# Performance work log

Measured on AMD Instinct MI355X. Metric: run time of the kernel, lower is better.

Reference implementation:

```python
import jax, jax.numpy as jnp
import numpy as np

N, L, D = 4, 2048, 1024
H_DIM, OUT_DIM = 1024, 1024


def setup_inputs() -> dict:
    key = jax.random.key(0)
    ks = jax.random.split(key, 7)
    scale = 0.02
    return {
        "x": jax.random.normal(ks[0], (N, L, D), dtype=jnp.float32),
        "Wq": jax.random.normal(ks[1], (D, H_DIM), dtype=jnp.float32) * scale,
        "bq": jnp.zeros((H_DIM,), dtype=jnp.float32),
        "Wk": jax.random.normal(ks[2], (D, H_DIM), dtype=jnp.float32) * scale,
        "bk": jnp.zeros((H_DIM,), dtype=jnp.float32),
        "Wv": jax.random.normal(ks[3], (D, OUT_DIM), dtype=jnp.float32) * scale,
        "bv": jnp.zeros((OUT_DIM,), dtype=jnp.float32),
    }


def reference(x, Wq, bq, Wk, bk, Wv, bv):
    # q,k: [N,L,h_dim], v: [N,L,out_dim]
    q = jnp.einsum("nld,dh->nlh", x, Wq) + bq
    k = jnp.einsum("nld,dh->nlh", x, Wk) + bk
    v = jnp.einsum("nld,do->nlo", x, Wv) + bv
    # scores: [N,L,L]
    qk = jnp.einsum("nlh,nmh->nlm", q, k)
    # NOTE: original scales by sqrt(qk.shape[-1]) == sqrt(L) (seq len), not sqrt(h_dim)
    seq_len = qk.shape[-1]
    s = jax.nn.softmax(qk / jnp.sqrt(jnp.asarray(seq_len, dtype=qk.dtype)), axis=-1)
    return jnp.einsum("nlm,nmo->nlo", s, v)
```

## Files before the change

### kernel.cpp

```cpp
#include <hip/hip_runtime.h>
#include <hip/hip_bf16.h>


typedef __attribute__((ext_vector_type(8))) short bf16x8;
typedef __attribute__((ext_vector_type(4))) float f32x4;

#define AS_G(p) ((__attribute__((address_space(1))) void*)(p))
#define AS_L(p) ((__attribute__((address_space(3))) void*)(p))

__device__ __forceinline__ unsigned short f2bf(float f) {
  unsigned int u = __float_as_uint(f);
  unsigned int lsb = (u >> 16) & 1u;
  u += 0x7fffu + lsb;
  return (unsigned short)(u >> 16);
}

__device__ __forceinline__ float bf2f(unsigned short h) {
  return __uint_as_float(((unsigned int)h) << 16);
}


template <int EPI>
__global__ __launch_bounds__(256) void gemm64(
    const unsigned short* __restrict__ A, const unsigned short* __restrict__ B,
    float* __restrict__ C, long long sA, long long sB, long long sC,
    int K, int lda, int ldb, int ldc,
    unsigned short* __restrict__ qb, unsigned short* __restrict__ kb,
    unsigned short* __restrict__ vt,
    const float* __restrict__ bq, const float* __restrict__ bk_,
    const float* __restrict__ bv)
{
  __shared__ unsigned short lA[128 * 64];
  __shared__ unsigned short lB[128 * 64];

  const int t = threadIdx.x;
  const int rowBase = blockIdx.y * 128;
  const int colBase = blockIdx.x * 128;
  A += (long long)blockIdx.z * sA;
  B += (long long)blockIdx.z * sB;

  const int l = t & 63;
  const int w = t >> 6;
  const int wrow = (w >> 1) * 64;
  const int wcol = (w & 1) * 64;
  const int q = l >> 4;
  const int r16 = l & 15;

  f32x4 acc[4][4] = {};

  const int r0 = t >> 3;
  const int goff = (((t & 7) ^ (r0 & 7)) << 3);

  for (int kt = 0; kt < K; kt += 64) {
    __syncthreads();
#pragma unroll
    for (int u = 0; u < 4; u++) {
      const int row = r0 + 32 * u;
      __builtin_amdgcn_global_load_lds(AS_G(A + (size_t)(rowBase + row) * lda + kt + goff),
                                       AS_L(lA + (t + 256 * u) * 8), 16, 0, 0);
      __builtin_amdgcn_global_load_lds(AS_G(B + (size_t)(colBase + row) * ldb + kt + goff),
                                       AS_L(lB + (t + 256 * u) * 8), 16, 0, 0);
    }
    __syncthreads();

#pragma unroll
    for (int ks = 0; ks < 2; ks++) {
      bf16x8 af[4], bfr[4];
#pragma unroll
      for (int i = 0; i < 4; i++) {
        const int s = ((ks * 4 + q) ^ (r16 & 7));
        af[i] = *(const bf16x8*)(lA + (wrow + i * 16 + r16) * 64 + s * 8);
      }
#pragma unroll
      for (int j = 0; j < 4; j++) {
        const int s = ((ks * 4 + q) ^ (r16 & 7));
        bfr[j] = *(const bf16x8*)(lB + (wcol + j * 16 + r16) * 64 + s * 8);
      }
#pragma unroll
      for (int i = 0; i < 4; i++)
#pragma unroll
        for (int j = 0; j < 4; j++)
          acc[i][j] = __builtin_amdgcn_mfma_f32_16x16x32_bf16(af[i], bfr[j], acc[i][j], 0, 0, 0);
    }
  }

  if (EPI == 0) {
    C += (long long)blockIdx.z * sC;
#pragma unroll
    for (int i = 0; i < 4; i++) {
#pragma unroll
      for (int r = 0; r < 4; r++) {
        int row = rowBase + wrow + i * 16 + q * 4 + r;
#pragma unroll
        for (int j = 0; j < 4; j++) {
          int col = colBase + wcol + j * 16 + r16;
          C[(size_t)row * ldc + col] = acc[i][j][r];
        }
      }
    }
  } else {
    const int seg = colBase >> 10;
    if (seg < 2) {
      unsigned short* dst = seg ? kb : qb;
      const float* bias = seg ? bk_ : bq;
      const int cb = colBase & 1023;
#pragma unroll
      for (int i = 0; i < 4; i++) {
#pragma unroll
        for (int r = 0; r < 4; r++) {
          int row = rowBase + wrow + i * 16 + q * 4 + r;
#pragma unroll
          for (int j = 0; j < 4; j++) {
            int col = cb + wcol + j * 16 + r16;
            dst[(size_t)row * 1024 + col] = f2bf(acc[i][j][r] + bias[col]);
          }
        }
      }
    } else {
      const int ob = colBase - 2048;
#pragma unroll
      for (int i = 0; i < 4; i++) {
        int posBase = rowBase + wrow + i * 16 + q * 4;
        int b = posBase >> 11;
        int pos = posBase & 2047;
#pragma unroll
        for (int j = 0; j < 4; j++) {
          int o = ob + wcol + j * 16 + r16;
          float bias = bv[o];
          ushort4 pk;
          pk.x = f2bf(acc[i][j][0] + bias);
          pk.y = f2bf(acc[i][j][1] + bias);
          pk.z = f2bf(acc[i][j][2] + bias);
          pk.w = f2bf(acc[i][j][3] + bias);
          *(ushort4*)(vt + ((size_t)((b << 10) + o) * 2048 + pos)) = pk;
        }
      }
    }
  }
}


__global__ __launch_bounds__(256) void cast_f32_to_bf16(
    const float* __restrict__ in, unsigned short* __restrict__ out, int n4)
{
  int i = blockIdx.x * 256 + threadIdx.x;
  if (i >= n4) return;
  float4 v = ((const float4*)in)[i];
  ushort4 o;
  o.x = f2bf(v.x); o.y = f2bf(v.y); o.z = f2bf(v.z); o.w = f2bf(v.w);
  ((ushort4*)out)[i] = o;
}


__global__ __launch_bounds__(256) void wtrans(
    const float* __restrict__ Wq, const float* __restrict__ Wk,
    const float* __restrict__ Wv, unsigned short* __restrict__ WT)
{
  __shared__ float tile[32][33];
  const float* in = blockIdx.z == 0 ? Wq : (blockIdx.z == 1 ? Wk : Wv);
  unsigned short* out = WT + (size_t)blockIdx.z * 1024 * 1024;
  const int bc = blockIdx.x * 32;
  const int br = blockIdx.y * 32;
  const int tx = threadIdx.x;
  const int ty = threadIdx.y;
#pragma unroll
  for (int i = 0; i < 4; i++)
    tile[ty + i * 8][tx] = in[(size_t)(br + ty + i * 8) * 1024 + bc + tx];
  __syncthreads();
#pragma unroll
  for (int i = 0; i < 4; i++)
    out[(size_t)(bc + ty + i * 8) * 1024 + br + tx] = f2bf(tile[tx][ty + i * 8]);
}


__global__ __launch_bounds__(256) void softmax_rows(
    const float* __restrict__ S, unsigned short* __restrict__ P, float scale)
{
  const size_t row = blockIdx.x;
  const float* s = S + row * 2048;
  unsigned short* p = P + row * 2048;
  const int t = threadIdx.x;

  float v[8];
  float m = -1e30f;
#pragma unroll
  for (int i = 0; i < 8; i++) {
    v[i] = s[t + i * 256];
    m = fmaxf(m, v[i]);
  }
#pragma unroll
  for (int off = 32; off >= 1; off >>= 1) m = fmaxf(m, __shfl_xor(m, off));
  __shared__ float redm[4];
  if ((t & 63) == 0) redm[t >> 6] = m;
  __syncthreads();
  m = fmaxf(fmaxf(redm[0], redm[1]), fmaxf(redm[2], redm[3]));

  float e[8];
  float sum = 0.f;
#pragma unroll
  for (int i = 0; i < 8; i++) {
    e[i] = __expf((v[i] - m) * scale);
    sum += e[i];
  }
#pragma unroll
  for (int off = 32; off >= 1; off >>= 1) sum += __shfl_xor(sum, off);
  __shared__ float reds[4];
  if ((t & 63) == 0) reds[t >> 6] = sum;
  __syncthreads();
  sum = reds[0] + reds[1] + reds[2] + reds[3];
  float inv = 1.0f / sum;
#pragma unroll
  for (int i = 0; i < 8; i++) p[t + i * 256] = f2bf(e[i] * inv);
}


extern "C" void kernel_launch(void* const* d_in, const int* in_sizes, int n_in,
                              void* d_out, int out_size, void* d_ws, size_t ws_size,
                              hipStream_t stream) {
  (void)in_sizes; (void)n_in; (void)out_size;

  const float* x  = (const float*)d_in[0];
  const float* Wq = (const float*)d_in[1];
  const float* bq = (const float*)d_in[2];
  const float* Wk = (const float*)d_in[3];
  const float* bk = (const float*)d_in[4];
  const float* Wv = (const float*)d_in[5];
  const float* bv = (const float*)d_in[6];
  float* out = (float*)d_out;

  const int Nb = 4, L = 2048, D = 1024, H = 1024, O = 1024;
  const int M = Nb * L;
  const int NQKV = 3 * H;

  char* ws = (char*)d_ws;
  size_t off = 0;
  unsigned short* xb = (unsigned short*)(ws + off); off += (size_t)M * D * 2;
  unsigned short* qb = (unsigned short*)(ws + off); off += (size_t)M * H * 2;
  unsigned short* kb = (unsigned short*)(ws + off); off += (size_t)M * H * 2;
  unsigned short* vt = (unsigned short*)(ws + off); off += (size_t)M * O * 2;
  unsigned short* WT = (unsigned short*)(ws + off); off += (size_t)NQKV * D * 2;
  float* S = (float*)(ws + off); off += (size_t)Nb * L * L * 4;
  unsigned short* P = qb;
  if (ws_size < off) return;

  dim3 blk256(256);

  cast_f32_to_bf16<<<(M * D / 4 + 255) / 256, blk256, 0, stream>>>(x, xb, M * D / 4);

  wtrans<<<dim3(32, 32, 3), dim3(32, 8), 0, stream>>>(Wq, Wk, Wv, WT);

  gemm64<2><<<dim3(NQKV / 128, M / 128, 1), blk256, 0, stream>>>(
      xb, WT, nullptr, 0, 0, 0, D, D, D, 0, qb, kb, vt, bq, bk, bv);

  gemm64<0><<<dim3(L / 128, L / 128, Nb), blk256, 0, stream>>>(
      qb, kb, S, (long long)L * H, (long long)L * H, (long long)L * L,
      H, H, H, L, nullptr, nullptr, nullptr, nullptr, nullptr, nullptr);

  softmax_rows<<<Nb * L, blk256, 0, stream>>>(S, P, 0.022097086912079608f);

  gemm64<0><<<dim3(O / 128, L / 128, Nb), blk256, 0, stream>>>(
      P, vt, out, (long long)L * L, (long long)O * L, (long long)L * O,
      L, L, L, O, nullptr, nullptr, nullptr, nullptr, nullptr, nullptr);
}
```

Baseline: 276.5 us.

## Fuse softmax exp into QK GEMM epilogue and defer normalization to PV GEMM

The QK^T GEMM epilogue now computes exp(score*scale) directly, writes bf16 unnormalized probabilities, and accumulates per-row sums with atomics. The PV GEMM epilogue divides each output row by its sum. This removes the fp32 score matrix round trip and the separate softmax kernel. In exchange it drops the max-subtraction, so large scores could overflow exp, and it adds atomic contention on the row sums.

```diff
diff --git a/kernel.cpp b/kernel.cpp
--- a/kernel.cpp
+++ b/kernel.cpp
@@ -23,12 +23,13 @@
 template <int EPI>
 __global__ __launch_bounds__(256) void gemm64(
     const unsigned short* __restrict__ A, const unsigned short* __restrict__ B,
-    float* __restrict__ C, long long sA, long long sB, long long sC,
+    float* __restrict__ Cf, long long sA, long long sB, long long sC,
     int K, int lda, int ldb, int ldc,
-    unsigned short* __restrict__ qb, unsigned short* __restrict__ kb,
-    unsigned short* __restrict__ vt,
-    const float* __restrict__ bq, const float* __restrict__ bk_,
-    const float* __restrict__ bv)
+    unsigned short* __restrict__ u0, unsigned short* __restrict__ u1,
+    unsigned short* __restrict__ u2,
+    const float* __restrict__ f0, const float* __restrict__ f1,
+    const float* __restrict__ f2,
+    float* __restrict__ rsum, float scale)
 {
   __shared__ unsigned short lA[128 * 64];
   __shared__ unsigned short lB[128 * 64];
@@ -84,25 +85,32 @@
     }
   }
 
-  if (EPI == 0) {
-    C += (long long)blockIdx.z * sC;
+  if (EPI == 1) {
+    unsigned short* p16 = u0 + (long long)blockIdx.z * sC;
+    float* rs = rsum + (long long)blockIdx.z * 2048;
 #pragma unroll
     for (int i = 0; i < 4; i++) {
 #pragma unroll
       for (int r = 0; r < 4; r++) {
         int row = rowBase + wrow + i * 16 + q * 4 + r;
+        float rowpart = 0.f;
 #pragma unroll
         for (int j = 0; j < 4; j++) {
           int col = colBase + wcol + j * 16 + r16;
-          C[(size_t)row * ldc + col] = acc[i][j][r];
-        }
-      }
-    }
-  } else {
+          float e = __expf(acc[i][j][r] * scale);
+          p16[(size_t)row * ldc + col] = f2bf(e);
+          rowpart += e;
+        }
+#pragma unroll
+        for (int m = 1; m < 16; m <<= 1) rowpart += __shfl_xor(rowpart, m);
+        if (r16 == 0) atomicAdd(rs + row, rowpart);
+      }
+    }
+  } else if (EPI == 2) {
     const int seg = colBase >> 10;
     if (seg < 2) {
-      unsigned short* dst = seg ? kb : qb;
-      const float* bias = seg ? bk_ : bq;
+      unsigned short* dst = seg ? u1 : u0;
+      const float* bias = seg ? f1 : f0;
       const int cb = colBase & 1023;
 #pragma unroll
       for (int i = 0; i < 4; i++) {
@@ -126,13 +134,29 @@
 #pragma unroll
         for (int j = 0; j < 4; j++) {
           int o = ob + wcol + j * 16 + r16;
-          float bias = bv[o];
+          float bias = f2[o];
           ushort4 pk;
           pk.x = f2bf(acc[i][j][0] + bias);
           pk.y = f2bf(acc[i][j][1] + bias);
           pk.z = f2bf(acc[i][j][2] + bias);
           pk.w = f2bf(acc[i][j][3] + bias);
-          *(ushort4*)(vt + ((size_t)((b << 10) + o) * 2048 + pos)) = pk;
+          *(ushort4*)(u2 + ((size_t)((b << 10) + o) * 2048 + pos)) = pk;
+        }
+      }
+    }
+  } else {
+    float* C = Cf + (long long)blockIdx.z * sC;
+    const float* rs = rsum + (long long)blockIdx.z * 2048;
+#pragma unroll
+    for (int i = 0; i < 4; i++) {
+#pragma unroll
+      for (int r = 0; r < 4; r++) {
+        int row = rowBase + wrow + i * 16 + q * 4 + r;
+        float inv = 1.0f / rs[row];
+#pragma unroll
+        for (int j = 0; j < 4; j++) {
+          int col = colBase + wcol + j * 16 + r16;
+          C[(size_t)row * ldc + col] = acc[i][j][r] * inv;
         }
       }
     }
@@ -141,9 +165,11 @@
 
 
 __global__ __launch_bounds__(256) void cast_f32_to_bf16(
-    const float* __restrict__ in, unsigned short* __restrict__ out, int n4)
+    const float* __restrict__ in, unsigned short* __restrict__ out, int n4,
+    float* __restrict__ rzero, int nz4)
 {
   int i = blockIdx.x * 256 + threadIdx.x;
+  if (i < nz4) ((float4*)rzero)[i] = make_float4(0.f, 0.f, 0.f, 0.f);
   if (i >= n4) return;
   float4 v = ((const float4*)in)[i];
   ushort4 o;
@@ -173,47 +199,6 @@
 }
 
 
-__global__ __launch_bounds__(256) void softmax_rows(
-    const float* __restrict__ S, unsigned short* __restrict__ P, float scale)
-{
-  const size_t row = blockIdx.x;
-  const float* s = S + row * 2048;
-  unsigned short* p = P + row * 2048;
-  const int t = threadIdx.x;
-
-  float v[8];
-  float m = -1e30f;
-#pragma unroll
-  for (int i = 0; i < 8; i++) {
-    v[i] = s[t + i * 256];
-    m = fmaxf(m, v[i]);
-  }
-#pragma unroll
-  for (int off = 32; off >= 1; off >>= 1) m = fmaxf(m, __shfl_xor(m, off));
-  __shared__ float redm[4];
-  if ((t & 63) == 0) redm[t >> 6] = m;
-  __syncthreads();
-  m = fmaxf(fmaxf(redm[0], redm[1]), fmaxf(redm[2], redm[3]));
-
-  float e[8];
-  float sum = 0.f;
-#pragma unroll
-  for (int i = 0; i < 8; i++) {
-    e[i] = __expf((v[i] - m) * scale);
-    sum += e[i];
-  }
-#pragma unroll
-  for (int off = 32; off >= 1; off >>= 1) sum += __shfl_xor(sum, off);
-  __shared__ float reds[4];
-  if ((t & 63) == 0) reds[t >> 6] = sum;
-  __syncthreads();
-  sum = reds[0] + reds[1] + reds[2] + reds[3];
-  float inv = 1.0f / sum;
-#pragma unroll
-  for (int i = 0; i < 8; i++) p[t + i * 256] = f2bf(e[i] * inv);
-}
-
-
 extern "C" void kernel_launch(void* const* d_in, const int* in_sizes, int n_in,
                               void* d_out, int out_size, void* d_ws, size_t ws_size,
                               hipStream_t stream) {
@@ -239,26 +224,30 @@
   unsigned short* kb = (unsigned short*)(ws + off); off += (size_t)M * H * 2;
   unsigned short* vt = (unsigned short*)(ws + off); off += (size_t)M * O * 2;
   unsigned short* WT = (unsigned short*)(ws + off); off += (size_t)NQKV * D * 2;
-  float* S = (float*)(ws + off); off += (size_t)Nb * L * L * 4;
-  unsigned short* P = qb;
+  unsigned short* P  = (unsigned short*)(ws + off); off += (size_t)Nb * L * L * 2;
+  float* rsum = (float*)(ws + off); off += (size_t)Nb * L * 4;
   if (ws_size < off) return;
 
   dim3 blk256(256);
 
-  cast_f32_to_bf16<<<(M * D / 4 + 255) / 256, blk256, 0, stream>>>(x, xb, M * D / 4);
+  cast_f32_to_bf16<<<(M * D / 4 + 255) / 256, blk256, 0, stream>>>(
+      x, xb, M * D / 4, rsum, Nb * L / 4);
 
   wtrans<<<dim3(32, 32, 3), dim3(32, 8), 0, stream>>>(Wq, Wk, Wv, WT);
 
   gemm64<2><<<dim3(NQKV / 128, M / 128, 1), blk256, 0, stream>>>(
-      xb, WT, nullptr, 0, 0, 0, D, D, D, 0, qb, kb, vt, bq, bk, bv);
-
-  gemm64<0><<<dim3(L / 128, L / 128, Nb), blk256, 0, stream>>>(
-      qb, kb, S, (long long)L * H, (long long)L * H, (long long)L * L,
-      H, H, H, L, nullptr, nullptr, nullptr, nullptr, nullptr, nullptr);
-
-  softmax_rows<<<Nb * L, blk256, 0, stream>>>(S, P, 0.022097086912079608f);
-
-  gemm64<0><<<dim3(O / 128, L / 128, Nb), blk256, 0, stream>>>(
+      xb, WT, nullptr, 0, 0, 0, D, D, D, 0,
+      qb, kb, vt, bq, bk, bv, nullptr, 0.f);
+
+  gemm64<1><<<dim3(L / 128, L / 128, Nb), blk256, 0, stream>>>(
+      qb, kb, nullptr, (long long)L * H, (long long)L * H, (long long)L * L,
+      H, H, H, L,
+      P, nullptr, nullptr, nullptr, nullptr, nullptr,
+      rsum, 0.022097086912079608f );
+
+  gemm64<3><<<dim3(O / 128, L / 128, Nb), blk256, 0, stream>>>(
       P, vt, out, (long long)L * L, (long long)O * L, (long long)L * O,
-      L, L, L, O, nullptr, nullptr, nullptr, nullptr, nullptr, nullptr);
-}
+      L, L, L, O,
+      nullptr, nullptr, nullptr, nullptr, nullptr, nullptr,
+      rsum, 0.f);
+}
```

New measurement: 271.8 us. About the same (-1.7%).
